# Optimization experiments

Measured on AMD Instinct MI355X. Metric: run time of the kernel, lower is better.

The kernel has to match this reference:

```python
import jax, jax.numpy as jnp
import numpy as np

IN, H, OUT, T = 512, 2048, 512, 8192


def setup_inputs() -> dict:
    key = jax.random.key(0)
    ks = jax.random.split(key, 9)
    s = 1.0 / np.sqrt(H).astype(np.float32)  # PyTorch LSTM/Linear init range
    u = lambda k, shape: jax.random.uniform(k, shape, jnp.float32, -s, s)
    return {
        "sequence": jax.random.normal(ks[0], (T, IN), jnp.float32),
        "W_ih": u(ks[1], (4 * H, IN)),
        "W_hh": u(ks[2], (4 * H, H)),
        "b_ih": u(ks[3], (4 * H,)),
        "b_hh": u(ks[4], (4 * H,)),
        "h0": jax.random.normal(ks[5], (H,), jnp.float32),  # module's random hidden init (batch=1 flattened)
        "c0": jax.random.normal(ks[6], (H,), jnp.float32),
        "W_lin": u(ks[7], (OUT, H)),
        "b_lin": u(ks[8], (OUT,)),
    }


def reference(sequence, W_ih, W_hh, b_ih, b_hh, h0, c0, W_lin, b_lin):
    # Precompute input contribution to gates for all timesteps in one GEMM: [T, 4H]
    x_gates = sequence @ W_ih.T + (b_ih + b_hh)

    def cell(carry, xg):
        h, c = carry
        g = xg + h @ W_hh.T                      # [4H]
        i, f, gg, o = jnp.split(g, 4)            # PyTorch gate order: i, f, g, o
        i = jax.nn.sigmoid(i)
        f = jax.nn.sigmoid(f)
        gg = jnp.tanh(gg)
        o = jax.nn.sigmoid(o)
        c = f * c + i * gg
        h = o * jnp.tanh(c)
        return (h, c), h

    (h_last, _), _ = jax.lax.scan(cell, (h0, c0), x_gates)
    # linear on every step then take last == linear on last hidden state
    pred = h_last @ W_lin.T + b_lin              # [OUT]
    return pred[None, :]                          # [1, OUT], matches prediction[-1]
```

## Files before the change

### kernel.cpp

```cpp
#include <hip/hip_runtime.h>
#include <hip/hip_bf16.h>
#include <stdint.h>



__device__ __forceinline__ uint32_t packbf(float a, float b) {
    uint32_t ua = __float_as_uint(a);
    uint32_t ub = __float_as_uint(b);
    ua = (ua + 0x7fffu + ((ua >> 16) & 1u)) >> 16;
    ub = (ub + 0x7fffu + ((ub >> 16) & 1u)) >> 16;
    return ua | (ub << 16);
}

__device__ __forceinline__ float dot2bf(uint32_t a, uint32_t b, float c) {
    float d;
    asm("v_dot2_f32_bf16 %0, %1, %2, %3" : "=v"(d) : "v"(a), "v"(b), "v"(c));
    return d;
}

__device__ __forceinline__ float sigm(float x) { return 1.f / (1.f + __expf(-x)); }
__device__ __forceinline__ float tanh_fast(float x) { return 1.f - 2.f / (1.f + __expf(2.f * x)); }

#define ALOAD(p) __hip_atomic_load((p), __ATOMIC_RELAXED, __HIP_MEMORY_SCOPE_AGENT)

__global__ __launch_bounds__(256) void init_hbuf(unsigned long long* hbuf) {
    int i = blockIdx.x * 256 + threadIdx.x;
    if (i < 2048) hbuf[i] = ~0ull;
}

__global__ __launch_bounds__(256, 1) void lstm_persist(const float* __restrict__ seq,
                                                       const float* __restrict__ Wih,
                                                       const float* __restrict__ Whh,
                                                       const float* __restrict__ bih,
                                                       const float* __restrict__ bhh,
                                                       const float* __restrict__ h0,
                                                       const float* __restrict__ c0,
                                                       unsigned long long* hbuf,
                                                       float* __restrict__ hf32) {
    const int b = blockIdx.x, tid = threadIdx.x;
    const int q = tid >> 6, lane = tid & 63;
    const int hb = b * 8;
    const int rb = (lane >> 2) & 1;
    const int myrow = hb + 2 * q + rb;

    uint32_t w[160];
#pragma unroll
    for (int c = 0; c < 8; c++) {
        const int R = (c >> 1) * 2048 + hb + 2 * q + (c & 1);
        const float2* rih = (const float2*)(Wih + (size_t)R * 512);
        const float2* rhh = (const float2*)(Whh + (size_t)R * 2048);
#pragma unroll
        for (int k = 0; k < 4; k++) {
            float2 v = rih[k * 64 + lane];
            w[c * 20 + k] = packbf(v.x, v.y);
        }
#pragma unroll
        for (int k = 4; k < 20; k++) {
            float2 v = rhh[(k - 4) * 64 + lane];
            w[c * 20 + k] = packbf(v.x, v.y);
        }
    }

    __shared__ uint32_t v_stage[2][1280];

    const float bi = bih[myrow] + bhh[myrow];
    const float bf_ = bih[2048 + myrow] + bhh[2048 + myrow];
    const float bg = bih[4096 + myrow] + bhh[4096 + myrow];
    const float bo = bih[6144 + myrow] + bhh[6144 + myrow];
    float c_state = c0[myrow];

    if (q == 0 && lane < 4) {
        float a = h0[hb + lane * 2], b2 = h0[hb + lane * 2 + 1];
        unsigned long long v = ((unsigned long long)packbf(a, b2) << 32);
        __hip_atomic_store(&hbuf[b * 4 + lane], v, __ATOMIC_RELAXED, __HIP_MEMORY_SCOPE_AGENT);
    }

    float2 xv = ((const float2*)seq)[tid];
    int gave_up = 0;

    for (int s = 1; s <= 8192; s++) {
        const int t = s - 1, bs = t & 1;
        v_stage[bs][tid] = packbf(xv.x, xv.y);
        if (s < 8192) xv = ((const float2*)(seq + (size_t)s * 512))[tid];

        if (!gave_up) {
            const unsigned long long* hp = hbuf + ((t & 1) << 10) + q * 256 + lane;
            uint32_t* vs = &v_stage[bs][256 + q * 256 + lane];
            const uint32_t want = (uint32_t)t;
            unsigned long long a0 = ALOAD(&hp[0]), a1 = ALOAD(&hp[64]),
                               a2 = ALOAD(&hp[128]), a3 = ALOAD(&hp[192]);
            int tries = 0;
            for (;;) {
                unsigned long long b0 = ALOAD(&hp[0]), b1 = ALOAD(&hp[64]),
                                   b2 = ALOAD(&hp[128]), b3 = ALOAD(&hp[192]);
                vs[0]   = (uint32_t)(a0 >> 32);
                vs[64]  = (uint32_t)(a1 >> 32);
                vs[128] = (uint32_t)(a2 >> 32);
                vs[192] = (uint32_t)(a3 >> 32);
                int ok = ((uint32_t)a0 == want) & ((uint32_t)a1 == want) &
                         ((uint32_t)a2 == want) & ((uint32_t)a3 == want);
                if (__all(ok)) break;
                a0 = ALOAD(&hp[0]); a1 = ALOAD(&hp[64]);
                a2 = ALOAD(&hp[128]); a3 = ALOAD(&hp[192]);
                vs[0]   = (uint32_t)(b0 >> 32);
                vs[64]  = (uint32_t)(b1 >> 32);
                vs[128] = (uint32_t)(b2 >> 32);
                vs[192] = (uint32_t)(b3 >> 32);
                ok = ((uint32_t)b0 == want) & ((uint32_t)b1 == want) &
                     ((uint32_t)b2 == want) & ((uint32_t)b3 == want);
                if (__all(ok)) break;
                if (++tries > (1 << 17)) { gave_up = 1; break; }
            }
        }
        __syncthreads();

        float acc[8] = {0.f, 0.f, 0.f, 0.f, 0.f, 0.f, 0.f, 0.f};
#pragma unroll
        for (int k = 0; k < 20; k++) {
            uint32_t hv = v_stage[bs][k * 64 + lane];
#pragma unroll
            for (int c = 0; c < 8; c++) acc[c] = dot2bf(w[c * 20 + k], hv, acc[c]);
        }

#pragma unroll
        for (int j = 0; j < 4; j++) {
            float lo = acc[j], hi = acc[j + 4];
            float sel = (lane & 1) ? lo : hi;
            float got = __shfl_xor(sel, 1, 64);
            acc[j] = ((lane & 1) ? hi : lo) + got;
        }
#pragma unroll
        for (int j = 0; j < 2; j++) {
            float lo = acc[j], hi = acc[j + 2];
            float sel = (lane & 2) ? lo : hi;
            float got = __shfl_xor(sel, 2, 64);
            acc[j] = ((lane & 2) ? hi : lo) + got;
        }
        {
            float lo = acc[0], hi = acc[1];
            float sel = (lane & 4) ? lo : hi;
            float got = __shfl_xor(sel, 4, 64);
            acc[0] = ((lane & 4) ? hi : lo) + got;
        }
        acc[0] += __shfl_xor(acc[0], 8, 64);
        acc[0] += __shfl_xor(acc[0], 16, 64);
        acc[0] += __shfl_xor(acc[0], 32, 64);

        const int base = lane & ~3;
        float gi = __shfl(acc[0], base, 64);
        float gg = __shfl(acc[0], base + 1, 64);
        float gf = __shfl(acc[0], base + 2, 64);
        float go = __shfl(acc[0], base + 3, 64);
        float i_ = sigm(gi + bi), f_ = sigm(gf + bf_), g_ = tanh_fast(gg + bg), o_ = sigm(go + bo);
        c_state = f_ * c_state + i_ * g_;
        float hval = o_ * tanh_fast(c_state);

        float h1 = __shfl(hval, 4, 64);
        if (lane == 0) {
            unsigned long long v = ((unsigned long long)packbf(hval, h1) << 32) | (uint32_t)s;
            __hip_atomic_store(&hbuf[((s & 1) << 10) + b * 4 + q], v,
                               __ATOMIC_RELAXED, __HIP_MEMORY_SCOPE_AGENT);
            if (s == 8192) { hf32[hb + 2 * q] = hval; hf32[hb + 2 * q + 1] = h1; }
        }
    }
}

__global__ __launch_bounds__(256) void final_linear(const float* __restrict__ hf,
                                                    const float* __restrict__ Wlin,
                                                    const float* __restrict__ blin,
                                                    float* __restrict__ out) {
    const int row = blockIdx.x * 4 + (threadIdx.x >> 6);
    const int lane = threadIdx.x & 63;
    float acc = 0.f;
#pragma unroll
    for (int it = 0; it < 8; it++) {
        int c = it * 256 + lane * 4;
        float4 wv = *(const float4*)&Wlin[(size_t)row * 2048 + c];
        float4 hv = *(const float4*)&hf[c];
        acc += wv.x * hv.x + wv.y * hv.y + wv.z * hv.z + wv.w * hv.w;
    }
#pragma unroll
    for (int off = 32; off; off >>= 1) acc += __shfl_xor(acc, off, 64);
    if (lane == 0) out[row] = acc + blin[row];
}

extern "C" void kernel_launch(void* const* d_in, const int* in_sizes, int n_in,
                              void* d_out, int out_size, void* d_ws, size_t ws_size,
                              hipStream_t stream) {
    const float* seq  = (const float*)d_in[0];
    const float* Wih  = (const float*)d_in[1];
    const float* Whh  = (const float*)d_in[2];
    const float* bih  = (const float*)d_in[3];
    const float* bhh  = (const float*)d_in[4];
    const float* h0   = (const float*)d_in[5];
    const float* c0   = (const float*)d_in[6];
    const float* Wlin = (const float*)d_in[7];
    const float* blin = (const float*)d_in[8];
    float* out = (float*)d_out;

    char* ws = (char*)d_ws;
    unsigned long long* hbuf = (unsigned long long*)ws;
    float* hf32 = (float*)(ws + 16384);

    init_hbuf<<<8, 256, 0, stream>>>(hbuf);
    lstm_persist<<<256, 256, 0, stream>>>(seq, Wih, Whh, bih, bhh, h0, c0, hbuf, hf32);
    final_linear<<<128, 256, 0, stream>>>(hf32, Wlin, blin, out);
}
```

Baseline: 17.47 ms.

## Use two-level aggregator barrier and compute input projection before waiting

Replaces per-block polling of all 1024 hidden-state slots with a two-level scheme. Wave 0 in each of the first 16 blocks polls a 64-slot slice of the state buffer and publishes a go-tag; every block then polls only the 16 go-tags before reading the full state once. The input-gate dot products now run in registers from prefetched inputs before the wait, which takes them off the serial critical path. The trade-off is an extra hop of cross-CU latency per step, in exchange for much less polling traffic on the shared buffer.

```diff
diff --git a/kernel.cpp b/kernel.cpp
--- a/kernel.cpp
+++ b/kernel.cpp
@@ -21,11 +21,13 @@
 __device__ __forceinline__ float sigm(float x) { return 1.f / (1.f + __expf(-x)); }
 __device__ __forceinline__ float tanh_fast(float x) { return 1.f - 2.f / (1.f + __expf(2.f * x)); }
 
-#define ALOAD(p) __hip_atomic_load((p), __ATOMIC_RELAXED, __HIP_MEMORY_SCOPE_AGENT)
-
-__global__ __launch_bounds__(256) void init_hbuf(unsigned long long* hbuf) {
+#define ALOAD(p)  __hip_atomic_load((p), __ATOMIC_RELAXED, __HIP_MEMORY_SCOPE_AGENT)
+#define ASTORE(p, v) __hip_atomic_store((p), (v), __ATOMIC_RELAXED, __HIP_MEMORY_SCOPE_AGENT)
+
+__global__ __launch_bounds__(256) void init_hbuf(unsigned long long* hbuf, uint32_t* gotag) {
     int i = blockIdx.x * 256 + threadIdx.x;
     if (i < 2048) hbuf[i] = ~0ull;
+    if (i < 128) gotag[i] = ~0u;
 }
 
 __global__ __launch_bounds__(256, 1) void lstm_persist(const float* __restrict__ seq,
@@ -36,6 +38,7 @@
                                                        const float* __restrict__ h0,
                                                        const float* __restrict__ c0,
                                                        unsigned long long* hbuf,
+                                                       uint32_t* gotag,
                                                        float* __restrict__ hf32) {
     const int b = blockIdx.x, tid = threadIdx.x;
     const int q = tid >> 6, lane = tid & 63;
@@ -61,65 +64,93 @@
         }
     }
 
-    __shared__ uint32_t v_stage[2][1280];
-
-    const float bi = bih[myrow] + bhh[myrow];
+    __shared__ uint32_t v_stage[2][1024];
+
+    const float bi  = bih[myrow] + bhh[myrow];
     const float bf_ = bih[2048 + myrow] + bhh[2048 + myrow];
-    const float bg = bih[4096 + myrow] + bhh[4096 + myrow];
-    const float bo = bih[6144 + myrow] + bhh[6144 + myrow];
+    const float bg  = bih[4096 + myrow] + bhh[4096 + myrow];
+    const float bo  = bih[6144 + myrow] + bhh[6144 + myrow];
     float c_state = c0[myrow];
 
     if (q == 0 && lane < 4) {
         float a = h0[hb + lane * 2], b2 = h0[hb + lane * 2 + 1];
         unsigned long long v = ((unsigned long long)packbf(a, b2) << 32);
-        __hip_atomic_store(&hbuf[b * 4 + lane], v, __ATOMIC_RELAXED, __HIP_MEMORY_SCOPE_AGENT);
-    }
-
-    float2 xv = ((const float2*)seq)[tid];
+        ASTORE(&hbuf[b * 4 + lane], v);
+    }
+
+    float2 xn[4];
+#pragma unroll
+    for (int k = 0; k < 4; k++) xn[k] = ((const float2*)seq)[k * 64 + lane];
+
     int gave_up = 0;
+    const int is_agg = (b < 16) && (q == 0);
 
     for (int s = 1; s <= 8192; s++) {
         const int t = s - 1, bs = t & 1;
-        v_stage[bs][tid] = packbf(xv.x, xv.y);
-        if (s < 8192) xv = ((const float2*)(seq + (size_t)s * 512))[tid];
-
-        if (!gave_up) {
-            const unsigned long long* hp = hbuf + ((t & 1) << 10) + q * 256 + lane;
-            uint32_t* vs = &v_stage[bs][256 + q * 256 + lane];
-            const uint32_t want = (uint32_t)t;
-            unsigned long long a0 = ALOAD(&hp[0]), a1 = ALOAD(&hp[64]),
-                               a2 = ALOAD(&hp[128]), a3 = ALOAD(&hp[192]);
+        const uint32_t want = (uint32_t)t;
+
+        float acc[8];
+        {
+            uint32_t x0 = packbf(xn[0].x, xn[0].y), x1 = packbf(xn[1].x, xn[1].y);
+            uint32_t x2 = packbf(xn[2].x, xn[2].y), x3 = packbf(xn[3].x, xn[3].y);
+#pragma unroll
+            for (int c = 0; c < 8; c++) {
+                float a0 = dot2bf(w[c * 20 + 0], x0, 0.f);
+                a0 = dot2bf(w[c * 20 + 1], x1, a0);
+                a0 = dot2bf(w[c * 20 + 2], x2, a0);
+                acc[c] = dot2bf(w[c * 20 + 3], x3, a0);
+            }
+        }
+        if (s < 8192) {
+            const float2* xp = (const float2*)(seq + (size_t)s * 512);
+#pragma unroll
+            for (int k = 0; k < 4; k++) xn[k] = xp[k * 64 + lane];
+        }
+
+        if (is_agg && !gave_up) {
+            const unsigned long long* ap = hbuf + (bs << 10) + b * 64 + lane;
+            unsigned long long a0 = ALOAD(ap);
             int tries = 0;
             for (;;) {
-                unsigned long long b0 = ALOAD(&hp[0]), b1 = ALOAD(&hp[64]),
-                                   b2 = ALOAD(&hp[128]), b3 = ALOAD(&hp[192]);
-                vs[0]   = (uint32_t)(a0 >> 32);
-                vs[64]  = (uint32_t)(a1 >> 32);
-                vs[128] = (uint32_t)(a2 >> 32);
-                vs[192] = (uint32_t)(a3 >> 32);
-                int ok = ((uint32_t)a0 == want) & ((uint32_t)a1 == want) &
-                         ((uint32_t)a2 == want) & ((uint32_t)a3 == want);
-                if (__all(ok)) break;
-                a0 = ALOAD(&hp[0]); a1 = ALOAD(&hp[64]);
-                a2 = ALOAD(&hp[128]); a3 = ALOAD(&hp[192]);
-                vs[0]   = (uint32_t)(b0 >> 32);
-                vs[64]  = (uint32_t)(b1 >> 32);
-                vs[128] = (uint32_t)(b2 >> 32);
-                vs[192] = (uint32_t)(b3 >> 32);
-                ok = ((uint32_t)b0 == want) & ((uint32_t)b1 == want) &
-                     ((uint32_t)b2 == want) & ((uint32_t)b3 == want);
-                if (__all(ok)) break;
+                unsigned long long b0 = ALOAD(ap);
+                if (__all((uint32_t)a0 == want)) break;
+                a0 = ALOAD(ap);
+                if (__all((uint32_t)b0 == want)) break;
                 if (++tries > (1 << 17)) { gave_up = 1; break; }
             }
+            if (lane == 0) ASTORE(&gotag[bs * 64 + b], want);
+        }
+
+        if (!gave_up) {
+            const uint32_t* gp = gotag + bs * 64 + (lane & 15);
+            uint32_t a0 = ALOAD(gp);
+            int tries = 0;
+            for (;;) {
+                uint32_t b0 = ALOAD(gp);
+                if (__all(a0 == want)) break;
+                a0 = ALOAD(gp);
+                if (__all(b0 == want)) break;
+                if (++tries > (1 << 17)) { gave_up = 1; break; }
+            }
+        }
+
+        {
+            const unsigned long long* hp = hbuf + (bs << 10) + q * 256 + lane;
+            unsigned long long v0 = ALOAD(&hp[0]),   v1 = ALOAD(&hp[64]);
+            unsigned long long v2 = ALOAD(&hp[128]), v3 = ALOAD(&hp[192]);
+            uint32_t* vs = &v_stage[bs][q * 256 + lane];
+            vs[0]   = (uint32_t)(v0 >> 32);
+            vs[64]  = (uint32_t)(v1 >> 32);
+            vs[128] = (uint32_t)(v2 >> 32);
+            vs[192] = (uint32_t)(v3 >> 32);
         }
         __syncthreads();
 
-        float acc[8] = {0.f, 0.f, 0.f, 0.f, 0.f, 0.f, 0.f, 0.f};
-#pragma unroll
-        for (int k = 0; k < 20; k++) {
+#pragma unroll
+        for (int k = 0; k < 16; k++) {
             uint32_t hv = v_stage[bs][k * 64 + lane];
 #pragma unroll
-            for (int c = 0; c < 8; c++) acc[c] = dot2bf(w[c * 20 + k], hv, acc[c]);
+            for (int c = 0; c < 8; c++) acc[c] = dot2bf(w[c * 20 + 4 + k], hv, acc[c]);
         }
 
 #pragma unroll
@@ -158,8 +189,7 @@
         float h1 = __shfl(hval, 4, 64);
         if (lane == 0) {
             unsigned long long v = ((unsigned long long)packbf(hval, h1) << 32) | (uint32_t)s;
-            __hip_atomic_store(&hbuf[((s & 1) << 10) + b * 4 + q], v,
-                               __ATOMIC_RELAXED, __HIP_MEMORY_SCOPE_AGENT);
+            ASTORE(&hbuf[((s & 1) << 10) + b * 4 + q], v);
             if (s == 8192) { hf32[hb + 2 * q] = hval; hf32[hb + 2 * q + 1] = h1; }
         }
     }
@@ -200,9 +230,10 @@
 
     char* ws = (char*)d_ws;
     unsigned long long* hbuf = (unsigned long long*)ws;
-    float* hf32 = (float*)(ws + 16384);
-
-    init_hbuf<<<8, 256, 0, stream>>>(hbuf);
-    lstm_persist<<<256, 256, 0, stream>>>(seq, Wih, Whh, bih, bhh, h0, c0, hbuf, hf32);
+    uint32_t* gotag = (uint32_t*)(ws + 16384);
+    float* hf32 = (float*)(ws + 16384 + 512);
+
+    init_hbuf<<<8, 256, 0, stream>>>(hbuf, gotag);
+    lstm_persist<<<256, 256, 0, stream>>>(seq, Wih, Whh, bih, bhh, h0, c0, hbuf, gotag, hf32);
     final_linear<<<128, 256, 0, stream>>>(hf32, Wlin, blin, out);
 }
```

After: 37.77 ms. 2.16x slower.
